# Optimization experiments

Hardware: AMD Instinct MI355X
Metric: run time of the kernel (lower is better)

Reference implementation:

```python
import jax, jax.numpy as jnp
import numpy as np

N_NODES = 100000


def _gcn_conv(x, W, b, row, col, norm, n):
    # PyG GCNConv: h = x @ W, then symmetric-normalized scatter-add, then bias
    h = x @ W                          # [N, out]
    msg = h[col] * norm[:, None]       # gather at source nodes, scale per-edge
    out = jax.ops.segment_sum(msg, row, num_segments=n)  # scatter-add to dest
    return out + b


def setup_inputs() -> dict:
    key = jax.random.key(0)
    k1, k2, k3, k4, k5, k6 = jax.random.split(key, 6)
    F_in, H, C = 128, 128, 64
    E = 1600000
    x = jax.random.normal(k1, (N_NODES, F_in), dtype=jnp.float32)
    edge_index = jax.random.randint(k2, (2, E), 0, N_NODES, dtype=jnp.int64)
    s1 = 1.0 / np.sqrt(F_in)
    s2 = 1.0 / np.sqrt(H)
    W1 = jax.random.uniform(k3, (F_in, H), jnp.float32, -s1, s1)
    b1 = jax.random.uniform(k4, (H,), jnp.float32, -s1, s1)
    W2 = jax.random.uniform(k5, (H, C), jnp.float32, -s2, s2)
    b2 = jax.random.uniform(k6, (C,), jnp.float32, -s2, s2)
    return {"x": x, "edge_index": edge_index, "W1": W1, "b1": b1, "W2": W2, "b2": b2}


def reference(x, edge_index, W1, b1, W2, b2):
    n = x.shape[0]
    # add self-loops (GCNConv default)
    loops = jnp.arange(n, dtype=edge_index.dtype)
    row = jnp.concatenate([edge_index[0], loops])  # destination
    col = jnp.concatenate([edge_index[1], loops])  # source
    # symmetric normalization deg^{-1/2}[row] * deg^{-1/2}[col]
    deg = jax.ops.segment_sum(jnp.ones_like(row, dtype=x.dtype), row, num_segments=n)
    dinv = jnp.where(deg > 0, jax.lax.rsqrt(deg), 0.0)
    norm = dinv[row] * dinv[col]       # [E+N]
    h = jax.nn.relu(_gcn_conv(x, W1, b1, row, col, norm, n))
    # dropout is identity in eval mode
    out = _gcn_conv(h, W2, b2, row, col, norm, n)
    return jax.nn.log_softmax(out, axis=1)
```

## Files before the change

### kernel.cpp

```cpp
#include <hip/hip_runtime.h>
#include <hip/hip_fp16.h>
#include <cstdint>
#include <cstddef>

#define TPB 256
#define NWIN 8
#define CAP 64

using half8 = __attribute__((ext_vector_type(8))) _Float16;
using f32x4 = __attribute__((ext_vector_type(4))) float;

__device__ inline int edge_at(const void* __restrict__ ei, int is64, long long idx) {
    return is64 ? (int)((const long long*)ei)[idx] : ((const int*)ei)[idx];
}

__global__ void k_setup(const long long* __restrict__ ei, int nCheck, int N,
                        int* __restrict__ flag,
                        const float* __restrict__ W1, const float* __restrict__ W2,
                        _Float16* __restrict__ wf1, _Float16* __restrict__ wf2,
                        int* __restrict__ cnt) {
    int b = blockIdx.x;
    if (b == 0) {
        __shared__ int bad;
        if (threadIdx.x == 0) bad = 0;
        __syncthreads();
        for (int i = threadIdx.x; i < nCheck; i += blockDim.x) {
            long long v = ei[i];
            if (v < 0 || v >= (long long)N) bad = 1;
        }
        __syncthreads();
        if (threadIdx.x == 0) *flag = bad ? 0 : 1;
    } else if (b <= 16) {
        int i = (b - 1) * TPB + threadIdx.x;
        int k  = i >> 5;
        int n0 = (i & 31) * 4;
        float4 w = ((const float4*)W1)[i];
        int ct = n0 >> 4, kb = k >> 5;
        int lane0 = ((k >> 3) & 3) * 16 + (n0 & 15);
        int j = k & 7;
        int base = ((ct * 4 + kb) * 64 + lane0) * 8 + j;
        wf1[base]      = (_Float16)w.x;
        wf1[base + 8]  = (_Float16)w.y;
        wf1[base + 16] = (_Float16)w.z;
        wf1[base + 24] = (_Float16)w.w;
    } else if (b <= 24) {
        int i = (b - 17) * TPB + threadIdx.x;
        int k  = i >> 4;
        int n0 = (i & 15) * 4;
        float4 w = ((const float4*)W2)[i];
        int ct = n0 >> 4, kb = k >> 5;
        int lane0 = ((k >> 3) & 3) * 16 + (n0 & 15);
        int j = k & 7;
        int base = ((ct * 4 + kb) * 64 + lane0) * 8 + j;
        wf2[base]      = (_Float16)w.x;
        wf2[base + 8]  = (_Float16)w.y;
        wf2[base + 16] = (_Float16)w.z;
        wf2[base + 24] = (_Float16)w.w;
    } else {
        int i = (b - 25) * TPB + threadIdx.x;
        if (i < N) cnt[i] = 0;
    }
}

__global__ __launch_bounds__(256)
void k_mega(const void* __restrict__ ei, const int* __restrict__ flag,
            int E, int winRows, int N,
            int* __restrict__ cnt, int* __restrict__ slots,
            const float* __restrict__ x, const half8* __restrict__ wf1,
            __half* __restrict__ xw1, int nFill, int nGemm) {
    __shared__ __align__(16) _Float16 Of[4][16 * 136];

    if ((int)blockIdx.x < nFill) {
        const int is64 = *flag;
        const int w = blockIdx.x & (NWIN - 1);
        const int lo = w * winRows, hi = lo + winRows;
        const int nChunks = (E + 1023) >> 10;
        const int stride = nFill / NWIN;
        for (int chunk = blockIdx.x / NWIN; chunk < nChunks; chunk += stride) {
            int base = (chunk << 10) + threadIdx.x * 4;
            if (base >= E) continue;
            int r[4], c[4];
            if (base + 3 < E) {
                if (is64) {
                    const long long* e64 = (const long long*)ei;
#pragma unroll
                    for (int k = 0; k < 4; ++k) {
                        r[k] = (int)e64[base + k];
                        c[k] = (int)e64[(long long)E + base + k];
                    }
                } else {
                    const int* e32 = (const int*)ei;
                    int4 rv = *(const int4*)(e32 + base);
                    int4 cv = *(const int4*)(e32 + E + base);
                    r[0] = rv.x; r[1] = rv.y; r[2] = rv.z; r[3] = rv.w;
                    c[0] = cv.x; c[1] = cv.y; c[2] = cv.z; c[3] = cv.w;
                }
            } else {
#pragma unroll
                for (int k = 0; k < 4; ++k) {
                    if (base + k < E) {
                        r[k] = edge_at(ei, is64, base + k);
                        c[k] = edge_at(ei, is64, (long long)E + base + k);
                    } else r[k] = -1;
                }
            }
            int pos[4];
#pragma unroll
            for (int k = 0; k < 4; ++k) {
                bool in = (r[k] >= lo && r[k] < hi);
                pos[k] = in ? atomicAdd(&cnt[r[k]], 1) : -1;
            }
#pragma unroll
            for (int k = 0; k < 4; ++k)
                if (pos[k] >= 0 && pos[k] < CAP)
                    slots[(size_t)r[k] * CAP + pos[k]] = c[k];
        }
    } else {
        const int gb = blockIdx.x - nFill;
        const int wave = threadIdx.x >> 6, lane = threadIdx.x & 63;
        const int m = lane & 15, quad = lane >> 4;
        const int nRowTiles = (N + 15) >> 4;

        for (int rt = gb * 4 + wave; rt < nRowTiles; rt += nGemm * 4) {
            const int row0 = rt * 16;
            const int arow = row0 + m;
            const bool rvalid = arow < N;
            const float* xrow = x + (size_t)(rvalid ? arow : 0) * 128;

            f32x4 acc[8];
#pragma unroll
            for (int ct = 0; ct < 8; ++ct) acc[ct] = (f32x4){0.f, 0.f, 0.f, 0.f};

#pragma unroll
            for (int kb = 0; kb < 4; ++kb) {
                const float4* ap = (const float4*)(xrow + kb * 32 + quad * 8);
                float4 a0 = ap[0], a1 = ap[1];
                half8 a;
                a[0] = (_Float16)a0.x; a[1] = (_Float16)a0.y;
                a[2] = (_Float16)a0.z; a[3] = (_Float16)a0.w;
                a[4] = (_Float16)a1.x; a[5] = (_Float16)a1.y;
                a[6] = (_Float16)a1.z; a[7] = (_Float16)a1.w;
#pragma unroll
                for (int ct = 0; ct < 8; ++ct) {
                    half8 b = wf1[(ct * 4 + kb) * 64 + lane];
                    acc[ct] = __builtin_amdgcn_mfma_f32_16x16x32_f16(a, b, acc[ct], 0, 0, 0);
                }
            }

            _Float16* myO = &Of[wave][0];
#pragma unroll
            for (int ct = 0; ct < 8; ++ct)
#pragma unroll
                for (int r = 0; r < 4; ++r)
                    myO[(quad * 4 + r) * 136 + ct * 16 + m] = (_Float16)acc[ct][r];
            int vr = N - row0; if (vr > 16) vr = 16;
            float4* dst = (float4*)(xw1 + (size_t)row0 * 128);
            for (int i = lane; i < vr * 16; i += 64) {
                int r = i >> 4, q = i & 15;
                dst[r * 16 + q] = *(const float4*)&myO[r * 136 + q * 8];
            }
        }
    }
}

__global__ __launch_bounds__(256)
void k_g1g2(const __half* __restrict__ xw1, const int* __restrict__ cnt,
            const int* __restrict__ slots, const float* __restrict__ bias,
            const half8* __restrict__ wf2, __half* __restrict__ xw2, int N) {
    __shared__ __align__(16) _Float16 Ht[16 * 136];
    __shared__ __align__(16) _Float16 Of[16 * 72];

    const int row0 = blockIdx.x * 16;
    const int local = threadIdx.x >> 4;
    const int lane16 = threadIdx.x & 15;
    const int node = row0 + local;

    {
        union { __half2 h2[4]; float4 f; } u;
        if (node < N) {
            int cn = cnt[node];
            int len = cn > CAP ? CAP : cn;
            float dvn = rsqrtf((float)cn + 1.0f);
            const int* sl = slots + (size_t)node * CAP;
            float acc[8];
            {
                float4 raw = *(const float4*)(xw1 + (size_t)node * 128 + lane16 * 8);
                const __half2* hp = (const __half2*)&raw;
#pragma unroll
                for (int k = 0; k < 4; ++k) {
                    float2 f = __half22float2(hp[k]);
                    acc[2 * k] = dvn * f.x; acc[2 * k + 1] = dvn * f.y;
                }
            }
            int j = 0;
            for (; j + 1 < len; j += 2) {
                int c0 = sl[j], c1 = sl[j + 1];
                float dv0 = rsqrtf((float)cnt[c0] + 1.0f);
                float dv1 = rsqrtf((float)cnt[c1] + 1.0f);
                float4 raw0 = *(const float4*)(xw1 + (size_t)c0 * 128 + lane16 * 8);
                float4 raw1 = *(const float4*)(xw1 + (size_t)c1 * 128 + lane16 * 8);
                const __half2* h0 = (const __half2*)&raw0;
                const __half2* h1 = (const __half2*)&raw1;
#pragma unroll
                for (int k = 0; k < 4; ++k) {
                    float2 f0 = __half22float2(h0[k]);
                    float2 f1 = __half22float2(h1[k]);
                    acc[2 * k]     = fmaf(dv0, f0.x, fmaf(dv1, f1.x, acc[2 * k]));
                    acc[2 * k + 1] = fmaf(dv0, f0.y, fmaf(dv1, f1.y, acc[2 * k + 1]));
                }
            }
            if (j < len) {
                int c = sl[j];
                float dv = rsqrtf((float)cnt[c] + 1.0f);
                float4 raw = *(const float4*)(xw1 + (size_t)c * 128 + lane16 * 8);
                const __half2* hp = (const __half2*)&raw;
#pragma unroll
                for (int k = 0; k < 4; ++k) {
                    float2 f = __half22float2(hp[k]);
                    acc[2 * k]     = fmaf(dv, f.x, acc[2 * k]);
                    acc[2 * k + 1] = fmaf(dv, f.y, acc[2 * k + 1]);
                }
            }
            float4 b01 = ((const float4*)bias)[lane16 * 2];
            float4 b23 = ((const float4*)bias)[lane16 * 2 + 1];
            float v[8];
            v[0] = b01.x + dvn * acc[0]; v[1] = b01.y + dvn * acc[1];
            v[2] = b01.z + dvn * acc[2]; v[3] = b01.w + dvn * acc[3];
            v[4] = b23.x + dvn * acc[4]; v[5] = b23.y + dvn * acc[5];
            v[6] = b23.z + dvn * acc[6]; v[7] = b23.w + dvn * acc[7];
#pragma unroll
            for (int k = 0; k < 4; ++k)
                u.h2[k] = __floats2half2_rn(fmaxf(v[2 * k], 0.f), fmaxf(v[2 * k + 1], 0.f));
        } else {
            u.f = make_float4(0.f, 0.f, 0.f, 0.f);
        }
        *(float4*)(Ht + local * 136 + lane16 * 8) = u.f;
    }
    __syncthreads();

    {
        const int wave = threadIdx.x >> 6, lane = threadIdx.x & 63;
        const int m = lane & 15, quad = lane >> 4;
        f32x4 acc = (f32x4){0.f, 0.f, 0.f, 0.f};
#pragma unroll
        for (int kb = 0; kb < 4; ++kb) {
            half8 a = *(const half8*)(Ht + m * 136 + kb * 32 + quad * 8);
            half8 b = wf2[(wave * 4 + kb) * 64 + lane];
            acc = __builtin_amdgcn_mfma_f32_16x16x32_f16(a, b, acc, 0, 0, 0);
        }
#pragma unroll
        for (int r = 0; r < 4; ++r)
            Of[(quad * 4 + r) * 72 + wave * 16 + m] = (_Float16)acc[r];
    }
    __syncthreads();
    {
        int vr = N - row0; if (vr > 16) vr = 16;
        float4* dst = (float4*)(xw2 + (size_t)row0 * 64);
        for (int i = threadIdx.x; i < vr * 8; i += TPB) {
            int r = i >> 3, q = i & 7;
            dst[r * 8 + q] = *(const float4*)&Of[r * 72 + q * 8];
        }
    }
}

__global__ void k_gather2_lsm(const __half* __restrict__ xws, const int* __restrict__ cnt,
                              const int* __restrict__ slots,
                              const float* __restrict__ bias, float* __restrict__ out, int N) {
    long long t = (long long)blockIdx.x * TPB + threadIdx.x;
    int node = (int)(t >> 4);
    int lane = (int)(t & 15);
    if (node >= N) return;
    int cn = cnt[node];
    int len = cn > CAP ? CAP : cn;
    float dvn = rsqrtf((float)cn + 1.0f);
    const int* sl = slots + (size_t)node * CAP;
    float a0, a1, a2, a3;
    {
        float2 raw = *(const float2*)(xws + (size_t)node * 64 + lane * 4);
        const __half2* hp = (const __half2*)&raw;
        float2 f0 = __half22float2(hp[0]), f1 = __half22float2(hp[1]);
        a0 = dvn * f0.x; a1 = dvn * f0.y; a2 = dvn * f1.x; a3 = dvn * f1.y;
    }
    int j = 0;
    for (; j + 1 < len; j += 2) {
        int c0 = sl[j], c1 = sl[j + 1];
        float dv0 = rsqrtf((float)cnt[c0] + 1.0f);
        float dv1 = rsqrtf((float)cnt[c1] + 1.0f);
        float2 raw0 = *(const float2*)(xws + (size_t)c0 * 64 + lane * 4);
        float2 raw1 = *(const float2*)(xws + (size_t)c1 * 64 + lane * 4);
        const __half2* h0 = (const __half2*)&raw0;
        const __half2* h1 = (const __half2*)&raw1;
        float2 f00 = __half22float2(h0[0]), f01 = __half22float2(h0[1]);
        float2 f10 = __half22float2(h1[0]), f11 = __half22float2(h1[1]);
        a0 = fmaf(dv0, f00.x, fmaf(dv1, f10.x, a0));
        a1 = fmaf(dv0, f00.y, fmaf(dv1, f10.y, a1));
        a2 = fmaf(dv0, f01.x, fmaf(dv1, f11.x, a2));
        a3 = fmaf(dv0, f01.y, fmaf(dv1, f11.y, a3));
    }
    if (j < len) {
        int c = sl[j];
        float dv = rsqrtf((float)cnt[c] + 1.0f);
        float2 raw = *(const float2*)(xws + (size_t)c * 64 + lane * 4);
        const __half2* hp = (const __half2*)&raw;
        float2 f0 = __half22float2(hp[0]), f1 = __half22float2(hp[1]);
        a0 = fmaf(dv, f0.x, a0); a1 = fmaf(dv, f0.y, a1);
        a2 = fmaf(dv, f1.x, a2); a3 = fmaf(dv, f1.y, a3);
    }
    float4 bb = ((const float4*)bias)[lane];
    float v0 = bb.x + dvn * a0, v1 = bb.y + dvn * a1;
    float v2 = bb.z + dvn * a2, v3 = bb.w + dvn * a3;

    float m = fmaxf(fmaxf(v0, v1), fmaxf(v2, v3));
#pragma unroll
    for (int off = 1; off < 16; off <<= 1) m = fmaxf(m, __shfl_xor(m, off));
    float s = expf(v0 - m) + expf(v1 - m) + expf(v2 - m) + expf(v3 - m);
#pragma unroll
    for (int off = 1; off < 16; off <<= 1) s += __shfl_xor(s, off);
    float ls = m + logf(s);
    ((float4*)(out + (size_t)node * 64))[lane] =
        make_float4(v0 - ls, v1 - ls, v2 - ls, v3 - ls);
}

extern "C" void kernel_launch(void* const* d_in, const int* in_sizes, int n_in,
                              void* d_out, int out_size, void* d_ws, size_t ws_size,
                              hipStream_t stream) {
    const float* x  = (const float*)d_in[0];
    const void*  ei = d_in[1];
    const float* W1 = (const float*)d_in[2];
    const float* b1 = (const float*)d_in[3];
    const float* W2 = (const float*)d_in[4];
    const float* b2 = (const float*)d_in[5];
    float* out = (float*)d_out;

    const int N = in_sizes[0] / 128;
    const int E = in_sizes[1] / 2;

    char* base = (char*)d_ws;
    size_t off = 0;
    auto alloc = [&](size_t bytes) { char* p = base + off; off = (off + bytes + 255) & ~(size_t)255; return p; };
    int*      flag  = (int*)alloc(sizeof(int));
    int*      cnt   = (int*)alloc((size_t)N * sizeof(int));
    _Float16* wf1   = (_Float16*)alloc(128 * 128 * sizeof(_Float16));
    _Float16* wf2   = (_Float16*)alloc(128 * 64 * sizeof(_Float16));
    int*      slots = (int*)alloc((size_t)N * CAP * sizeof(int));
    __half*   xw1   = (__half*)alloc((size_t)N * 128 * sizeof(__half));
    __half*   xw2   = (__half*)alloc((size_t)N * 64 * sizeof(__half));
    (void)ws_size;

    const int winRows = (N + NWIN - 1) / NWIN;
    const int nFill = 1024, nGemm = 512;
    const int nodeTiles = (N + 15) / 16;

    int nCheck = (2 * E < 512) ? 2 * E : 512;
    k_setup<<<25 + (N + TPB - 1) / TPB, TPB, 0, stream>>>(
        (const long long*)ei, nCheck, N, flag, W1, W2, wf1, wf2, cnt);

    k_mega<<<nFill + nGemm, TPB, 0, stream>>>(ei, flag, E, winRows, N, cnt, slots,
                                              x, (const half8*)wf1, xw1, nFill, nGemm);

    k_g1g2<<<nodeTiles, TPB, 0, stream>>>(xw1, cnt, slots, b1, (const half8*)wf2, xw2, N);

    {
        long long t = (long long)N * 16;
        k_gather2_lsm<<<(int)((t + TPB - 1) / TPB), TPB, 0, stream>>>(xw2, cnt, slots, b2, out, N);
    }
}
```

Before: 291.9 us.

## Pre-decode int64 edge list into compact int2 pairs and unroll gathers by four

The setup kernel now converts the edge list, int64 or int32, into a compact int2 (dst,src) array once. The fill phase, which runs 8 window passes over all edges, then reads 8 bytes per edge instead of 16 from the int64 input. Both gather kernels also unroll their neighbor loops from two to four, using an int4 load of slot indices to expose more memory-level parallelism. The cost is an extra write and read of the pairs array, plus a per-block int64 range check repeated in every decode block.

```diff
diff --git a/kernel.cpp b/kernel.cpp
--- a/kernel.cpp
+++ b/kernel.cpp
@@ -10,28 +10,13 @@
 using half8 = __attribute__((ext_vector_type(8))) _Float16;
 using f32x4 = __attribute__((ext_vector_type(4))) float;
 
-__device__ inline int edge_at(const void* __restrict__ ei, int is64, long long idx) {
-    return is64 ? (int)((const long long*)ei)[idx] : ((const int*)ei)[idx];
-}
-
-__global__ void k_setup(const long long* __restrict__ ei, int nCheck, int N,
-                        int* __restrict__ flag,
+__global__ void k_setup(const void* __restrict__ ei, int E, int N,
                         const float* __restrict__ W1, const float* __restrict__ W2,
                         _Float16* __restrict__ wf1, _Float16* __restrict__ wf2,
-                        int* __restrict__ cnt) {
+                        int* __restrict__ cnt, int2* __restrict__ pairs, int nCnt) {
     int b = blockIdx.x;
-    if (b == 0) {
-        __shared__ int bad;
-        if (threadIdx.x == 0) bad = 0;
-        __syncthreads();
-        for (int i = threadIdx.x; i < nCheck; i += blockDim.x) {
-            long long v = ei[i];
-            if (v < 0 || v >= (long long)N) bad = 1;
-        }
-        __syncthreads();
-        if (threadIdx.x == 0) *flag = bad ? 0 : 1;
-    } else if (b <= 16) {
-        int i = (b - 1) * TPB + threadIdx.x;
+    if (b < 16) {
+        int i = b * TPB + threadIdx.x;
         int k  = i >> 5;
         int n0 = (i & 31) * 4;
         float4 w = ((const float4*)W1)[i];
@@ -43,8 +28,8 @@
         wf1[base + 8]  = (_Float16)w.y;
         wf1[base + 16] = (_Float16)w.z;
         wf1[base + 24] = (_Float16)w.w;
-    } else if (b <= 24) {
-        int i = (b - 17) * TPB + threadIdx.x;
+    } else if (b < 24) {
+        int i = (b - 16) * TPB + threadIdx.x;
         int k  = i >> 4;
         int n0 = (i & 15) * 4;
         float4 w = ((const float4*)W2)[i];
@@ -56,22 +41,46 @@
         wf2[base + 8]  = (_Float16)w.y;
         wf2[base + 16] = (_Float16)w.z;
         wf2[base + 24] = (_Float16)w.w;
+    } else if (b < 24 + nCnt) {
+        int i = (b - 24) * TPB + threadIdx.x;
+        if (i < N) cnt[i] = 0;
     } else {
-        int i = (b - 25) * TPB + threadIdx.x;
-        if (i < N) cnt[i] = 0;
+        __shared__ int bad;
+        if (threadIdx.x == 0) bad = 0;
+        __syncthreads();
+        if (threadIdx.x < 256) {
+            long long v = ((const long long*)ei)[threadIdx.x];
+            if (v < 0 || v >= (long long)N) bad = 1;
+        }
+        __syncthreads();
+        int is64 = !bad;
+        int base = ((b - 24 - nCnt) * TPB + threadIdx.x) * 4;
+        if (base >= E) return;
+        if (is64) {
+            const long long* e64 = (const long long*)ei;
+#pragma unroll
+            for (int k = 0; k < 4; ++k)
+                if (base + k < E)
+                    pairs[base + k] = make_int2((int)e64[base + k],
+                                                (int)e64[(long long)E + base + k]);
+        } else {
+            const int* e32 = (const int*)ei;
+#pragma unroll
+            for (int k = 0; k < 4; ++k)
+                if (base + k < E)
+                    pairs[base + k] = make_int2(e32[base + k], e32[E + base + k]);
+        }
     }
 }
 
 __global__ __launch_bounds__(256)
-void k_mega(const void* __restrict__ ei, const int* __restrict__ flag,
-            int E, int winRows, int N,
+void k_mega(const int2* __restrict__ pairs, int E, int winRows, int N,
             int* __restrict__ cnt, int* __restrict__ slots,
             const float* __restrict__ x, const half8* __restrict__ wf1,
             __half* __restrict__ xw1, int nFill, int nGemm) {
     __shared__ __align__(16) _Float16 Of[4][16 * 136];
 
     if ((int)blockIdx.x < nFill) {
-        const int is64 = *flag;
         const int w = blockIdx.x & (NWIN - 1);
         const int lo = w * winRows, hi = lo + winRows;
         const int nChunks = (E + 1023) >> 10;
@@ -79,41 +88,27 @@
         for (int chunk = blockIdx.x / NWIN; chunk < nChunks; chunk += stride) {
             int base = (chunk << 10) + threadIdx.x * 4;
             if (base >= E) continue;
-            int r[4], c[4];
+            int2 p[4];
             if (base + 3 < E) {
-                if (is64) {
-                    const long long* e64 = (const long long*)ei;
-#pragma unroll
-                    for (int k = 0; k < 4; ++k) {
-                        r[k] = (int)e64[base + k];
-                        c[k] = (int)e64[(long long)E + base + k];
-                    }
-                } else {
-                    const int* e32 = (const int*)ei;
-                    int4 rv = *(const int4*)(e32 + base);
-                    int4 cv = *(const int4*)(e32 + E + base);
-                    r[0] = rv.x; r[1] = rv.y; r[2] = rv.z; r[3] = rv.w;
-                    c[0] = cv.x; c[1] = cv.y; c[2] = cv.z; c[3] = cv.w;
-                }
+                const int4* p4 = (const int4*)(pairs + base);
+                int4 u0 = p4[0], u1 = p4[1];
+                p[0] = make_int2(u0.x, u0.y); p[1] = make_int2(u0.z, u0.w);
+                p[2] = make_int2(u1.x, u1.y); p[3] = make_int2(u1.z, u1.w);
             } else {
 #pragma unroll
-                for (int k = 0; k < 4; ++k) {
-                    if (base + k < E) {
-                        r[k] = edge_at(ei, is64, base + k);
-                        c[k] = edge_at(ei, is64, (long long)E + base + k);
-                    } else r[k] = -1;
-                }
+                for (int k = 0; k < 4; ++k)
+                    p[k] = (base + k < E) ? pairs[base + k] : make_int2(-1, -1);
             }
             int pos[4];
 #pragma unroll
             for (int k = 0; k < 4; ++k) {
-                bool in = (r[k] >= lo && r[k] < hi);
-                pos[k] = in ? atomicAdd(&cnt[r[k]], 1) : -1;
+                bool in = (p[k].x >= lo && p[k].x < hi);
+                pos[k] = in ? atomicAdd(&cnt[p[k].x], 1) : -1;
             }
 #pragma unroll
             for (int k = 0; k < 4; ++k)
                 if (pos[k] >= 0 && pos[k] < CAP)
-                    slots[(size_t)r[k] * CAP + pos[k]] = c[k];
+                    slots[(size_t)p[k].x * CAP + pos[k]] = p[k].y;
         }
     } else {
         const int gb = blockIdx.x - nFill;
@@ -193,23 +188,33 @@
                 }
             }
             int j = 0;
-            for (; j + 1 < len; j += 2) {
-                int c0 = sl[j], c1 = sl[j + 1];
-                float dv0 = rsqrtf((float)cnt[c0] + 1.0f);
-                float dv1 = rsqrtf((float)cnt[c1] + 1.0f);
-                float4 raw0 = *(const float4*)(xw1 + (size_t)c0 * 128 + lane16 * 8);
-                float4 raw1 = *(const float4*)(xw1 + (size_t)c1 * 128 + lane16 * 8);
+            for (; j + 3 < len; j += 4) {
+                int4 cc = *(const int4*)(sl + j);
+                float dv0 = rsqrtf((float)cnt[cc.x] + 1.0f);
+                float dv1 = rsqrtf((float)cnt[cc.y] + 1.0f);
+                float dv2 = rsqrtf((float)cnt[cc.z] + 1.0f);
+                float dv3 = rsqrtf((float)cnt[cc.w] + 1.0f);
+                float4 raw0 = *(const float4*)(xw1 + (size_t)cc.x * 128 + lane16 * 8);
+                float4 raw1 = *(const float4*)(xw1 + (size_t)cc.y * 128 + lane16 * 8);
+                float4 raw2 = *(const float4*)(xw1 + (size_t)cc.z * 128 + lane16 * 8);
+                float4 raw3 = *(const float4*)(xw1 + (size_t)cc.w * 128 + lane16 * 8);
                 const __half2* h0 = (const __half2*)&raw0;
                 const __half2* h1 = (const __half2*)&raw1;
+                const __half2* h2 = (const __half2*)&raw2;
+                const __half2* h3 = (const __half2*)&raw3;
 #pragma unroll
                 for (int k = 0; k < 4; ++k) {
                     float2 f0 = __half22float2(h0[k]);
                     float2 f1 = __half22float2(h1[k]);
-                    acc[2 * k]     = fmaf(dv0, f0.x, fmaf(dv1, f1.x, acc[2 * k]));
-                    acc[2 * k + 1] = fmaf(dv0, f0.y, fmaf(dv1, f1.y, acc[2 * k + 1]));
+                    float2 f2 = __half22float2(h2[k]);
+                    float2 f3 = __half22float2(h3[k]);
+                    acc[2 * k]     = fmaf(dv0, f0.x, fmaf(dv1, f1.x,
+                                     fmaf(dv2, f2.x, fmaf(dv3, f3.x, acc[2 * k]))));
+                    acc[2 * k + 1] = fmaf(dv0, f0.y, fmaf(dv1, f1.y,
+                                     fmaf(dv2, f2.y, fmaf(dv3, f3.y, acc[2 * k + 1]))));
                 }
             }
-            if (j < len) {
+            for (; j < len; ++j) {
                 int c = sl[j];
                 float dv = rsqrtf((float)cnt[c] + 1.0f);
                 float4 raw = *(const float4*)(xw1 + (size_t)c * 128 + lane16 * 8);
@@ -282,22 +287,30 @@
         a0 = dvn * f0.x; a1 = dvn * f0.y; a2 = dvn * f1.x; a3 = dvn * f1.y;
     }
     int j = 0;
-    for (; j + 1 < len; j += 2) {
-        int c0 = sl[j], c1 = sl[j + 1];
-        float dv0 = rsqrtf((float)cnt[c0] + 1.0f);
-        float dv1 = rsqrtf((float)cnt[c1] + 1.0f);
-        float2 raw0 = *(const float2*)(xws + (size_t)c0 * 64 + lane * 4);
-        float2 raw1 = *(const float2*)(xws + (size_t)c1 * 64 + lane * 4);
+    for (; j + 3 < len; j += 4) {
+        int4 cc = *(const int4*)(sl + j);
+        float dv0 = rsqrtf((float)cnt[cc.x] + 1.0f);
+        float dv1 = rsqrtf((float)cnt[cc.y] + 1.0f);
+        float dv2 = rsqrtf((float)cnt[cc.z] + 1.0f);
+        float dv3 = rsqrtf((float)cnt[cc.w] + 1.0f);
+        float2 raw0 = *(const float2*)(xws + (size_t)cc.x * 64 + lane * 4);
+        float2 raw1 = *(const float2*)(xws + (size_t)cc.y * 64 + lane * 4);
+        float2 raw2 = *(const float2*)(xws + (size_t)cc.z * 64 + lane * 4);
+        float2 raw3 = *(const float2*)(xws + (size_t)cc.w * 64 + lane * 4);
         const __half2* h0 = (const __half2*)&raw0;
         const __half2* h1 = (const __half2*)&raw1;
+        const __half2* h2 = (const __half2*)&raw2;
+        const __half2* h3 = (const __half2*)&raw3;
         float2 f00 = __half22float2(h0[0]), f01 = __half22float2(h0[1]);
         float2 f10 = __half22float2(h1[0]), f11 = __half22float2(h1[1]);
-        a0 = fmaf(dv0, f00.x, fmaf(dv1, f10.x, a0));
-        a1 = fmaf(dv0, f00.y, fmaf(dv1, f10.y, a1));
-        a2 = fmaf(dv0, f01.x, fmaf(dv1, f11.x, a2));
-        a3 = fmaf(dv0, f01.y, fmaf(dv1, f11.y, a3));
-    }
-    if (j < len) {
+        float2 f20 = __half22float2(h2[0]), f21 = __half22float2(h2[1]);
+        float2 f30 = __half22float2(h3[0]), f31 = __half22float2(h3[1]);
+        a0 = fmaf(dv0, f00.x, fmaf(dv1, f10.x, fmaf(dv2, f20.x, fmaf(dv3, f30.x, a0))));
+        a1 = fmaf(dv0, f00.y, fmaf(dv1, f10.y, fmaf(dv2, f20.y, fmaf(dv3, f30.y, a1))));
+        a2 = fmaf(dv0, f01.x, fmaf(dv1, f11.x, fmaf(dv2, f21.x, fmaf(dv3, f31.x, a2))));
+        a3 = fmaf(dv0, f01.y, fmaf(dv1, f11.y, fmaf(dv2, f21.y, fmaf(dv3, f31.y, a3))));
+    }
+    for (; j < len; ++j) {
         int c = sl[j];
         float dv = rsqrtf((float)cnt[c] + 1.0f);
         float2 raw = *(const float2*)(xws + (size_t)c * 64 + lane * 4);
@@ -338,10 +351,10 @@
     char* base = (char*)d_ws;
     size_t off = 0;
     auto alloc = [&](size_t bytes) { char* p = base + off; off = (off + bytes + 255) & ~(size_t)255; return p; };
-    int*      flag  = (int*)alloc(sizeof(int));
     int*      cnt   = (int*)alloc((size_t)N * sizeof(int));
     _Float16* wf1   = (_Float16*)alloc(128 * 128 * sizeof(_Float16));
     _Float16* wf2   = (_Float16*)alloc(128 * 64 * sizeof(_Float16));
+    int2*     pairs = (int2*)alloc((size_t)E * sizeof(int2));
     int*      slots = (int*)alloc((size_t)N * CAP * sizeof(int));
     __half*   xw1   = (__half*)alloc((size_t)N * 128 * sizeof(__half));
     __half*   xw2   = (__half*)alloc((size_t)N * 64 * sizeof(__half));
@@ -350,12 +363,13 @@
     const int winRows = (N + NWIN - 1) / NWIN;
     const int nFill = 1024, nGemm = 512;
     const int nodeTiles = (N + 15) / 16;
-
-    int nCheck = (2 * E < 512) ? 2 * E : 512;
-    k_setup<<<25 + (N + TPB - 1) / TPB, TPB, 0, stream>>>(
-        (const long long*)ei, nCheck, N, flag, W1, W2, wf1, wf2, cnt);
-
-    k_mega<<<nFill + nGemm, TPB, 0, stream>>>(ei, flag, E, winRows, N, cnt, slots,
+    const int nCnt = (N + TPB - 1) / TPB;
+    const int nDec = (E + TPB * 4 - 1) / (TPB * 4);
+
+    k_setup<<<24 + nCnt + nDec, TPB, 0, stream>>>(ei, E, N, W1, W2, wf1, wf2,
+                                                  cnt, pairs, nCnt);
+
+    k_mega<<<nFill + nGemm, TPB, 0, stream>>>(pairs, E, winRows, N, cnt, slots,
                                               x, (const half8*)wf1, xw1, nFill, nGemm);
 
     k_g1g2<<<nodeTiles, TPB, 0, stream>>>(xw1, cnt, slots, b1, (const half8*)wf2, xw2, N);
```

Result: no change. 287.3 us, median of 2 (-1.6%).
